# Performance work log

Measured on AMD Instinct MI355X. Metric: run time of the kernel, lower is better.

Reference implementation:

```python
import jax, jax.numpy as jnp
import numpy as np

N_NODES = 50000
N_HYPEREDGES = 10000
N_INC = 800000  # incidences (edges in the bipartite node-hyperedge graph)
D = 128
NEG_SLOPE = 0.2


def segment_softmax(logits, seg, num_segments):
    # numerically stable softmax within segments (grouped by seg)
    m = jax.ops.segment_max(logits, seg, num_segments=num_segments)
    e = jnp.exp(logits - m[seg])
    s = jax.ops.segment_sum(e, seg, num_segments=num_segments)
    return e / s[seg]


def safe_inv(d):
    return jnp.where(d > 0, 1.0 / d, 0.0)


def setup_inputs() -> dict:
    key = jax.random.key(0)
    ks = jax.random.split(key, 8)
    x = jax.random.normal(ks[0], (N_NODES, D), dtype=jnp.float32)
    idx0 = jax.random.randint(ks[1], (N_INC,), 0, N_NODES)          # node ids
    idx1 = jax.random.randint(ks[2], (N_INC,), 0, N_HYPEREDGES)     # hyperedge ids
    hyperedge_index = jnp.stack([idx0, idx1], axis=0).astype(jnp.int64)
    hyperedge_weight = jnp.ones((N_HYPEREDGES,), dtype=jnp.float32)
    sc = 1.0 / np.sqrt(D)
    W_lin = jax.random.normal(ks[3], (D, D), dtype=jnp.float32) * sc
    W_lin2 = jax.random.normal(ks[4], (D, D), dtype=jnp.float32) * sc
    W_lin3 = jax.random.normal(ks[5], (D, D), dtype=jnp.float32) * sc
    att = jax.random.normal(ks[6], (1, 1, 2 * D), dtype=jnp.float32) * sc
    att2 = jax.random.normal(ks[7], (1, 1, 2 * D), dtype=jnp.float32) * sc
    return {"x": x, "hyperedge_index": hyperedge_index,
            "hyperedge_weight": hyperedge_weight,
            "W_lin": W_lin, "W_lin2": W_lin2, "W_lin3": W_lin3,
            "att": att, "att2": att2}


def reference(x, hyperedge_index, hyperedge_weight, W_lin, W_lin2, W_lin3, att, att2):
    N, M = N_NODES, N_HYPEREDGES
    H, F = 1, D
    idx0 = hyperedge_index[0]  # node side  [E]
    idx1 = hyperedge_index[1]  # hyperedge side [E]

    # Hyperedge(): mean-style aggregation of node features into hyperedges
    ones_e = jnp.ones_like(idx1, dtype=x.dtype)
    Binv = safe_inv(jax.ops.segment_sum(ones_e, idx1, num_segments=M))  # [M]
    he0 = jax.ops.segment_sum(x[idx0], idx1, num_segments=M) * Binv[:, None]  # [M,D]

    # linear projections
    xl = (x @ W_lin).reshape(N, H, F)      # [N,H,F]
    hl = (he0 @ W_lin2).reshape(M, H, F)   # [M,H,F]

    # first attention: node-gathered vs hyperedge-gathered, softmax grouped by node
    x_i = xl[idx0]                          # [E,H,F]
    x_j = hl[idx1]                          # [E,H,F]
    alpha = (jnp.concatenate([x_i, x_j], axis=-1) * att).sum(-1)  # [E,H]
    alpha = jax.nn.leaky_relu(alpha, NEG_SLOPE)
    alpha = segment_softmax(alpha, idx0, N)

    # degree normalizations
    Dinv = safe_inv(jax.ops.segment_sum(hyperedge_weight[idx1], idx0, num_segments=N))  # [N]

    # propagate node -> hyperedge: out_e[e] = sum Binv[e]*alpha*x[node]
    msg1 = Binv[idx1][:, None, None] * alpha[:, :, None] * x_i  # [E,H,F]
    out_e = jax.ops.segment_sum(msg1, idx1, num_segments=M)     # [M,H,F]

    # second attention with lin3-transformed hyperedge features
    he2 = (out_e.reshape(M, H * F) @ W_lin3).reshape(M, H, F)
    x_j2 = he2[idx1]
    alpha2 = (jnp.concatenate([x_i, x_j2], axis=-1) * att2).sum(-1)  # [E,H]
    alpha2 = jax.nn.leaky_relu(alpha2, NEG_SLOPE)
    alpha2 = segment_softmax(alpha2, idx0, N)

    # propagate hyperedge -> node: out_n[n] = sum Dinv[n]*alpha2*out_e[hyperedge]
    msg2 = Dinv[idx0][:, None, None] * alpha2[:, :, None] * out_e[idx1]  # [E,H,F]
    out_n = jax.ops.segment_sum(msg2, idx0, num_segments=N)              # [N,H,F]

    return out_n.reshape(N, H * F)
```

## Files before the change

kernel.cpp:

```cpp
#include <hip/hip_runtime.h>
#include <math.h>

#define DF 128
#define TILE 8192
#define CAPA 8192
#define CAPB 10240
typedef unsigned int uint;
typedef __attribute__((ext_vector_type(8))) short bf16x8;
typedef __attribute__((ext_vector_type(4))) float f32x4;

__device__ __forceinline__ float leaky(float s){ return s > 0.f ? s : 0.2f*s; }

__device__ __forceinline__ uint bfr(float f){
    uint u = __float_as_uint(f);
    return (u + 0x7fffu + ((u >> 16) & 1u)) >> 16;
}
__device__ __forceinline__ uint bf2(float a, float b){ return bfr(a) | (bfr(b) << 16); }
__device__ __forceinline__ float blo(uint v){ return __uint_as_float(v << 16); }
__device__ __forceinline__ float bhi(uint v){ return __uint_as_float(v & 0xffff0000u); }

__device__ __forceinline__ uint fenc(float f){
    uint u = __float_as_uint(f);
    return (u & 0x80000000u) ? ~u : (u | 0x80000000u);
}
__device__ __forceinline__ float fdec(uint k){
    return (k & 0x80000000u) ? __uint_as_float(k ^ 0x80000000u) : __uint_as_float(~k);
}

__device__ __forceinline__ void load_edge(const void* raw, int is64, int E, int e,
                                          int& n, int& m){
    if (is64){
        const long long* p = (const long long*)raw;
        n = (int)p[e]; m = (int)p[(long long)E + e];
    } else {
        const int* p = (const int*)raw;
        n = p[e]; m = p[E + e];
    }
}

__global__ __launch_bounds__(256) void prep(
        const uint* __restrict__ raw, int* __restrict__ ctrl,
        int* __restrict__ gcurA, int* __restrict__ gcurB,
        const float* __restrict__ W1, const float* __restrict__ W2,
        const float* __restrict__ W3,
        const float* __restrict__ att, const float* __restrict__ att2,
        float* __restrict__ w2a, float* __restrict__ v1,
        float* __restrict__ v2, float* __restrict__ v3,
        uint* __restrict__ W1t, int E)
{
    int t = threadIdx.x;
    int bid = blockIdx.x;
    if (bid == 0){
        __shared__ int cnt;
        gcurA[t] = t*CAPA;
        gcurB[t] = t*CAPB;
        if (t == 0){ cnt = 0; ctrl[1] = 0; ctrl[2] = 0; }
        __syncthreads();
        int nz = 0;
        for (int i = 0; i < 4; i++){
            int w = 2*(t*4 + i) + 1;
            if (w < 2*E) nz += (raw[w] != 0u);
        }
        atomicAdd(&cnt, nz);
        __syncthreads();
        if (t == 0) ctrl[0] = (cnt == 0) ? 1 : 0;
    } else if (bid == 1){
        int d = t & 127;
        const float* W = (t < 128) ? W2 : W1;
        const float* a = (t < 128) ? (att + 128) : att;
        float s = 0.f;
        for (int f = 0; f < 128; f++) s += W[d*128 + f]*a[f];
        if (t < 128) w2a[d] = s; else v1[d] = s;
    } else if (bid == 2){
        __shared__ float sw3a[128];
        int d = t & 127;
        const float* W = (t < 128) ? W1 : W3;
        const float* a = (t < 128) ? att2 : (att2 + 128);
        float s = 0.f;
        for (int f = 0; f < 128; f++) s += W[d*128 + f]*a[f];
        if (t < 128) v2[d] = s; else sw3a[d] = s;
        __syncthreads();
        if (t < 128){
            float s2 = 0.f;
            for (int f = 0; f < 128; f++) s2 += W1[t*128 + f]*sw3a[f];
            v3[t] = s2;
        }
    } else {
        int base = (bid - 3)*1024;
        for (int p = base + t; p < base + 1024; p += 256){
            int f = p >> 6, dh = p & 63;
            W1t[p] = bf2(W1[(2*dh)*128 + f], W1[(2*dh + 1)*128 + f]);
        }
    }
}

__global__ __launch_bounds__(512) void scatter_gemm(
        const void* __restrict__ raw, const int* __restrict__ ctrl,
        int* __restrict__ gcurA, int* __restrict__ gcurB,
        uint* __restrict__ bktA, uint* __restrict__ bktB,
        const float* __restrict__ X, const uint* __restrict__ W1t,
        const float* __restrict__ w2a, const float* __restrict__ v1,
        const float* __restrict__ v2, const float* __restrict__ v3,
        uint* __restrict__ xlb, float* __restrict__ a1x, float* __restrict__ a2x,
        float* __restrict__ px, float* __restrict__ pxl,
        int E, int N, int SC)
{
    __shared__ char smem[73728];
    int t = threadIdx.x;
    int bid = blockIdx.x;

    if (bid < SC){
        uint* stA = (uint*)smem;
        uint* stB = (uint*)(smem + 32768);
        int*  hA  = (int*)(smem + 65536);
        int*  scA = hA + 256; int* cuA = hA + 512; int* bA = hA + 768;
        int*  hB  = hA + 1024; int* scB = hA + 1280; int* cuB = hA + 1536; int* bB = hA + 1792;
        if (t < 256){ hA[t] = 0; hB[t] = 0; }
        __syncthreads();
        int tb = bid*TILE;
        int cnt = min(TILE, E - tb);
        int is64 = ctrl[0];
        for (int i = t; i < cnt; i += 512){
            int n, m; load_edge(raw, is64, E, tb + i, n, m);
            atomicAdd(&hA[n >> 8], 1);
            atomicAdd(&hB[m >> 6], 1);
        }
        __syncthreads();
        if (t < 256){ scA[t] = hA[t]; scB[t] = hB[t]; }
        __syncthreads();
        for (int off = 1; off < 256; off <<= 1){
            int vA = 0, vB = 0;
            if (t < 256 && t >= off){ vA = scA[t - off]; vB = scB[t - off]; }
            __syncthreads();
            if (t < 256){ scA[t] += vA; scB[t] += vB; }
            __syncthreads();
        }
        if (t < 256){
            scA[t] -= hA[t]; scB[t] -= hB[t];
            cuA[t] = scA[t]; cuB[t] = scB[t];
            bA[t] = atomicAdd(&gcurA[t], hA[t]);
            bB[t] = atomicAdd(&gcurB[t], hB[t]);
        }
        __syncthreads();
        for (int i = t; i < cnt; i += 512){
            int n, m; load_edge(raw, is64, E, tb + i, n, m);
            int pA = atomicAdd(&cuA[n >> 8], 1);
            stA[pA] = ((uint)n << 14) | (uint)m;
            int pB = atomicAdd(&cuB[m >> 6], 1);
            stB[pB] = ((uint)m << 16) | (uint)n;
        }
        __syncthreads();
        for (int p = t; p < cnt; p += 512){
            uint v = stA[p]; int b = (int)(v >> 22);
            bktA[bA[b] + (p - scA[b])] = v;
            uint w = stB[p]; int c = (int)(w >> 22);
            bktB[bB[c] + (p - scB[c])] = w;
        }
    } else {
        char* lds = smem;
        int lane = t & 63, wv = t >> 6;
        int row0 = (bid - SC)*128;
        {
            const uint4* g = (const uint4*)W1t;
            #pragma unroll
            for (int i = 0; i < 4; i++){
                int u = i*512 + t;
                int col = u >> 4;
                uint4 v = g[u];
                *(uint4*)(lds + 32768 + ((u*16) ^ ((col & 7) << 4))) = v;
            }
        }
        {
            int cg = t & 31;
            float4 c_px = ((const float4*)w2a)[cg];
            float4 c_a1 = ((const float4*)v1 )[cg];
            float4 c_a2 = ((const float4*)v2 )[cg];
            float4 c_pl = ((const float4*)v3 )[cg];
            #pragma unroll
            for (int i = 0; i < 8; i++){
                int idx = i*512 + t;
                int rl = idx >> 5;
                int row = row0 + rl;
                float4 xv = make_float4(0.f, 0.f, 0.f, 0.f);
                if (row < N) xv = ((const float4*)X)[(size_t)row*32 + cg];
                uint2 pk; pk.x = bf2(xv.x, xv.y); pk.y = bf2(xv.z, xv.w);
                *(uint2*)(lds + rl*256 + ((cg*8) ^ ((rl & 7) << 4))) = pk;
                float d0 = xv.x*c_px.x + xv.y*c_px.y + xv.z*c_px.z + xv.w*c_px.w;
                float d1 = xv.x*c_a1.x + xv.y*c_a1.y + xv.z*c_a1.z + xv.w*c_a1.w;
                float d2 = xv.x*c_a2.x + xv.y*c_a2.y + xv.z*c_a2.z + xv.w*c_a2.w;
                float d3 = xv.x*c_pl.x + xv.y*c_pl.y + xv.z*c_pl.z + xv.w*c_pl.w;
                #pragma unroll
                for (int off = 16; off > 0; off >>= 1){
                    d0 += __shfl_xor(d0, off); d1 += __shfl_xor(d1, off);
                    d2 += __shfl_xor(d2, off); d3 += __shfl_xor(d3, off);
                }
                if (cg == 0 && row < N){
                    px[row] = d0; a1x[row] = d1; a2x[row] = d2; pxl[row] = d3;
                }
            }
        }
        __syncthreads();
        f32x4 acc[8];
        #pragma unroll
        for (int i = 0; i < 8; i++) acc[i] = (f32x4){0.f, 0.f, 0.f, 0.f};
        int arow = wv*16 + (lane & 15);
        int aswz = (arow & 7) << 4;
        int bswz = (lane & 7) << 4;
        #pragma unroll
        for (int ks = 0; ks < 4; ks++){
            int au16 = ((lane >> 4) + ks*4)*16;
            bf16x8 af = *(const bf16x8*)(lds + arow*256 + (au16 ^ aswz));
            #pragma unroll
            for (int nf = 0; nf < 8; nf++){
                int bcol = nf*16 + (lane & 15);
                bf16x8 bf = *(const bf16x8*)(lds + 32768 + bcol*256 + (au16 ^ bswz));
                acc[nf] = __builtin_amdgcn_mfma_f32_16x16x32_bf16(af, bf, acc[nf], 0, 0, 0);
            }
        }
        __syncthreads();
        #pragma unroll
        for (int nf = 0; nf < 8; nf++){
            #pragma unroll
            for (int reg = 0; reg < 4; reg++){
                int rl = wv*16 + (lane >> 4)*4 + reg;
                int col = nf*16 + (lane & 15);
                *(unsigned short*)(lds + rl*256 + ((col*2) ^ ((rl & 7) << 4))) =
                    (unsigned short)bfr(acc[nf][reg]);
            }
        }
        __syncthreads();
        #pragma unroll
        for (int j = 0; j < 4; j++){
            int unit = j*64 + lane;
            int rl = wv*16 + (unit >> 4);
            int uu = unit & 15;
            uint4 v = *(const uint4*)(lds + rl*256 + ((uu*16) ^ ((rl & 7) << 4)));
            int grow = row0 + rl;
            if (grow < N) ((uint4*)xlb)[(size_t)grow*16 + uu] = v;
        }
    }
}

__global__ __launch_bounds__(256) void csr_edge(
        const uint* __restrict__ bktB, const int* __restrict__ gcurB,
        int* __restrict__ adj1, int2* __restrict__ rg1,
        const float* __restrict__ px, float* __restrict__ a1h,
        uint* __restrict__ g1key, int M)
{
    __shared__ int h[64], sc[64], cu[64];
    __shared__ float fsum[64];
    int t = threadIdx.x;
    int b = blockIdx.x;
    int sb = b*CAPB;
    int total = gcurB[b] - sb;
    int kb = b << 6;
    if (t < 64){ h[t] = 0; fsum[t] = 0.f; }
    __syncthreads();
    const uint* src = bktB + sb;
    for (int i = t; i < total; i += 256)
        atomicAdd(&h[(int)(src[i] >> 16) - kb], 1);
    __syncthreads();
    if (t < 64) sc[t] = h[t];
    __syncthreads();
    for (int off = 1; off < 64; off <<= 1){
        int v = (t < 64 && t >= off) ? sc[t - off] : 0;
        __syncthreads();
        if (t < 64) sc[t] += v;
        __syncthreads();
    }
    if (t < 64){ sc[t] -= h[t]; cu[t] = sc[t]; }
    __syncthreads();
    for (int i = t; i < total; i += 256){
        uint v = src[i];
        int k = (int)(v >> 16) - kb;
        int pos = atomicAdd(&cu[k], 1);
        int n = (int)(v & 0xFFFFu);
        adj1[sb + pos] = n;
        atomicAdd(&fsum[k], px[n]);
    }
    __syncthreads();
    if (t < 64){
        int key = kb + t;
        float av = -3.4e38f;
        if (key < M){
            av = (h[t] > 0) ? fsum[t]/(float)h[t] : 0.f;
            rg1[key] = make_int2(sb + sc[t], sb + sc[t] + h[t]);
            a1h[key] = av;
        }
        #pragma unroll
        for (int off = 32; off > 0; off >>= 1)
            av = fmaxf(av, __shfl_xor(av, off));
        if (t == 0) atomicMax(g1key, fenc(av));
    }
}

__global__ __launch_bounds__(256) void csr_node(
        const uint* __restrict__ bktA, const int* __restrict__ gcurA,
        int* __restrict__ adj0, int2* __restrict__ rg0,
        const float* __restrict__ a1x, const float* __restrict__ a1h,
        const float* __restrict__ hw, const float* __restrict__ pxl,
        const uint* __restrict__ g1key, uint* __restrict__ g2key,
        float4* __restrict__ pk1, float* __restrict__ Dinv, int N)
{
    __shared__ int h[256], sc[256], cu[256];
    __shared__ uint sm[CAPA];
    __shared__ float wmax[4];
    int t = threadIdx.x;
    int b = blockIdx.x;
    int sb = b*CAPA;
    int total = gcurA[b] - sb;
    int kb = b << 8;
    float G1 = fdec(*g1key);
    h[t] = 0;
    __syncthreads();
    const uint* src = bktA + sb;
    for (int i = t; i < total; i += 256)
        atomicAdd(&h[(int)(src[i] >> 14) - kb], 1);
    __syncthreads();
    sc[t] = h[t];
    __syncthreads();
    for (int off = 1; off < 256; off <<= 1){
        int v = (t >= off) ? sc[t - off] : 0;
        __syncthreads();
        sc[t] += v;
        __syncthreads();
    }
    sc[t] -= h[t];
    cu[t] = sc[t];
    __syncthreads();
    for (int i = t; i < total; i += 256){
        uint v = src[i];
        int k = (int)(v >> 14) - kb;
        int pos = atomicAdd(&cu[k], 1);
        sm[pos] = v & 0x3FFFu;
    }
    __syncthreads();
    for (int i = t; i < total; i += 256) adj0[sb + i] = (int)sm[i];
    int key = kb + t;
    float pl = (key < N) ? pxl[key] : 0.f;
    if (key < N){
        int deg = h[t], beg = sc[t];
        rg0[key] = make_int2(sb + beg, sb + beg + deg);
        float ax = a1x[key];
        float mx = leaky(ax + G1);
        float se = 0.f, wsum = 0.f;
        for (int j = 0; j < deg; j++){
            int m = (int)sm[beg + j];
            wsum += hw[m];
            se += expf(leaky(ax + a1h[m]) - mx);
        }
        pk1[key] = make_float4(ax, mx, (deg > 0) ? 1.f/se : 0.f, pl);
        Dinv[key] = (wsum > 0.f) ? 1.f/wsum : 0.f;
    }
    float pv = pl;
    #pragma unroll
    for (int off = 32; off > 0; off >>= 1) pv = fmaxf(pv, __shfl_xor(pv, off));
    if ((t & 63) == 0) wmax[t >> 6] = pv;
    __syncthreads();
    if (t == 0){
        float bm = fmaxf(fmaxf(wmax[0], wmax[1]), fmaxf(wmax[2], wmax[3]));
        atomicMax(g2key, fenc(fmaxf(bm, 0.f)));
    }
}

__global__ __launch_bounds__(256) void agg_oute(
    const int2* __restrict__ rg1, const int* __restrict__ adj1,
    const float4* __restrict__ pk1, const float* __restrict__ a1h,
    const uint* __restrict__ xlb, uint* __restrict__ outeb,
    float* __restrict__ a2h, int M)
{
    __shared__ float part[2][132];
    int t = threadIdx.x;
    int wv = t >> 6, lane = t & 63;
    int slot = wv >> 1, half = wv & 1;
    int m = blockIdx.x*2 + slot;
    int sub = lane >> 4, cg = lane & 15;
    const uint4* x4p = (const uint4*)xlb;
    float acc[8] = {0,0,0,0,0,0,0,0};
    float sca = 0.f;
    float binv = 0.f;
    if (m < M){
        int2 r = rg1[m];
        int b = r.x, e = r.y, deg = e - b;
        binv = deg > 0 ? 1.f/(float)deg : 0.f;
        float ah = a1h[m];
        int hl = (deg + 1) >> 1;
        int hb = b + half*hl;
        int he = min(e, hb + hl);
        for (int base = hb; base < he; base += 64){
            int cnt = min(64, he - base);
            int n = 0; float al = 0.f;
            if (lane < cnt){
                n = adj1[base + lane];
                float4 g = pk1[n];
                al = expf(leaky(g.x + ah) - g.y) * g.z;
                sca += al * g.w;
            }
            int t4 = 0;
            for (; t4 + 8 <= cnt; t4 += 8){
                int   nb0 = __shfl(n,  t4 + sub);
                float ab0 = __shfl(al, t4 + sub);
                int   nb1 = __shfl(n,  t4 + 4 + sub);
                float ab1 = __shfl(al, t4 + 4 + sub);
                uint4 v0 = x4p[(size_t)nb0*16 + cg];
                uint4 v1 = x4p[(size_t)nb1*16 + cg];
                acc[0] += ab0*blo(v0.x); acc[1] += ab0*bhi(v0.x);
                acc[2] += ab0*blo(v0.y); acc[3] += ab0*bhi(v0.y);
                acc[4] += ab0*blo(v0.z); acc[5] += ab0*bhi(v0.z);
                acc[6] += ab0*blo(v0.w); acc[7] += ab0*bhi(v0.w);
                acc[0] += ab1*blo(v1.x); acc[1] += ab1*bhi(v1.x);
                acc[2] += ab1*blo(v1.y); acc[3] += ab1*bhi(v1.y);
                acc[4] += ab1*blo(v1.z); acc[5] += ab1*bhi(v1.z);
                acc[6] += ab1*blo(v1.w); acc[7] += ab1*bhi(v1.w);
            }
            for (; t4 < cnt; t4 += 4){
                int   nb = __shfl(n,  t4 + sub);
                float ab = __shfl(al, t4 + sub);
                uint4 v = x4p[(size_t)nb*16 + cg];
                acc[0] += ab*blo(v.x); acc[1] += ab*bhi(v.x);
                acc[2] += ab*blo(v.y); acc[3] += ab*bhi(v.y);
                acc[4] += ab*blo(v.z); acc[5] += ab*bhi(v.z);
                acc[6] += ab*blo(v.w); acc[7] += ab*bhi(v.w);
            }
        }
        #pragma unroll
        for (int i = 0; i < 8; i++){
            acc[i] += __shfl_xor(acc[i], 32);
            acc[i] += __shfl_xor(acc[i], 16);
        }
        #pragma unroll
        for (int off = 32; off > 0; off >>= 1) sca += __shfl_xor(sca, off);
    }
    if (half == 1 && lane < 16){
        #pragma unroll
        for (int i = 0; i < 8; i++) part[slot][cg*8 + i] = acc[i];
        if (lane == 0) part[slot][128] = sca;
    }
    __syncthreads();
    if (half == 0 && m < M && lane < 16){
        uint4 w;
        w.x = bf2(binv*(acc[0] + part[slot][cg*8+0]), binv*(acc[1] + part[slot][cg*8+1]));
        w.y = bf2(binv*(acc[2] + part[slot][cg*8+2]), binv*(acc[3] + part[slot][cg*8+3]));
        w.z = bf2(binv*(acc[4] + part[slot][cg*8+4]), binv*(acc[5] + part[slot][cg*8+5]));
        w.w = bf2(binv*(acc[6] + part[slot][cg*8+6]), binv*(acc[7] + part[slot][cg*8+7]));
        ((uint4*)outeb)[(size_t)m*16 + cg] = w;
        if (lane == 0) a2h[m] = binv*(sca + part[slot][128]);
    }
}

__global__ __launch_bounds__(256) void agg_outn(
    const int2* __restrict__ rg0, const int* __restrict__ adj0,
    const float* __restrict__ a2x, const float* __restrict__ a2h,
    const float* __restrict__ Dinv, const uint* __restrict__ outeb,
    const uint* __restrict__ g2key, float* __restrict__ out, int N)
{
    int n = blockIdx.x*4 + (threadIdx.x >> 6);
    int lane = threadIdx.x & 63;
    if (n >= N) return;
    int2 r = rg0[n];
    int b = r.x, e = r.y;
    float ax = a2x[n];
    float mx = leaky(ax + fdec(*g2key));
    int sub = lane >> 4, cg = lane & 15;
    const uint4* o4p = (const uint4*)outeb;
    float acc[8] = {0,0,0,0,0,0,0,0};
    float sa = 0.f;
    for (int base = b; base < e; base += 64){
        int cnt = min(64, e - base);
        int m = 0; float al = 0.f;
        if (lane < cnt){
            m = adj0[base + lane];
            al = expf(leaky(ax + a2h[m]) - mx);
            sa += al;
        }
        int t4 = 0;
        for (; t4 + 8 <= cnt; t4 += 8){
            int   mb0 = __shfl(m,  t4 + sub);
            float ab0 = __shfl(al, t4 + sub);
            int   mb1 = __shfl(m,  t4 + 4 + sub);
            float ab1 = __shfl(al, t4 + 4 + sub);
            uint4 v0 = o4p[(size_t)mb0*16 + cg];
            uint4 v1 = o4p[(size_t)mb1*16 + cg];
            acc[0] += ab0*blo(v0.x); acc[1] += ab0*bhi(v0.x);
            acc[2] += ab0*blo(v0.y); acc[3] += ab0*bhi(v0.y);
            acc[4] += ab0*blo(v0.z); acc[5] += ab0*bhi(v0.z);
            acc[6] += ab0*blo(v0.w); acc[7] += ab0*bhi(v0.w);
            acc[0] += ab1*blo(v1.x); acc[1] += ab1*bhi(v1.x);
            acc[2] += ab1*blo(v1.y); acc[3] += ab1*bhi(v1.y);
            acc[4] += ab1*blo(v1.z); acc[5] += ab1*bhi(v1.z);
            acc[6] += ab1*blo(v1.w); acc[7] += ab1*bhi(v1.w);
        }
        for (; t4 < cnt; t4 += 4){
            int   mb = __shfl(m,  t4 + sub);
            float ab = __shfl(al, t4 + sub);
            uint4 v = o4p[(size_t)mb*16 + cg];
            acc[0] += ab*blo(v.x); acc[1] += ab*bhi(v.x);
            acc[2] += ab*blo(v.y); acc[3] += ab*bhi(v.y);
            acc[4] += ab*blo(v.z); acc[5] += ab*bhi(v.z);
            acc[6] += ab*blo(v.w); acc[7] += ab*bhi(v.w);
        }
    }
    #pragma unroll
    for (int off = 32; off > 0; off >>= 1) sa += __shfl_xor(sa, off);
    #pragma unroll
    for (int i = 0; i < 8; i++){
        acc[i] += __shfl_xor(acc[i], 32);
        acc[i] += __shfl_xor(acc[i], 16);
    }
    float scale = (sa > 0.f) ? Dinv[n]/sa : 0.f;
    if (lane < 16){
        float4 o0 = make_float4(scale*acc[0], scale*acc[1], scale*acc[2], scale*acc[3]);
        float4 o1 = make_float4(scale*acc[4], scale*acc[5], scale*acc[6], scale*acc[7]);
        ((float4*)out)[(size_t)n*32 + cg*2]     = o0;
        ((float4*)out)[(size_t)n*32 + cg*2 + 1] = o1;
    }
}

extern "C" void kernel_launch(void* const* d_in, const int* in_sizes, int n_in,
                              void* d_out, int out_size, void* d_ws, size_t ws_size,
                              hipStream_t stream){
    const float* x    = (const float*)d_in[0];
    const void*  hidx = d_in[1];
    const float* hw   = (const float*)d_in[2];
    const float* W1   = (const float*)d_in[3];
    const float* W2   = (const float*)d_in[4];
    const float* W3   = (const float*)d_in[5];
    const float* att  = (const float*)d_in[6];
    const float* att2 = (const float*)d_in[7];
    float* out = (float*)d_out;

    const int N = in_sizes[0] / DF;
    const int E = in_sizes[1] / 2;
    const int M = in_sizes[2];

    char* ws = (char*)d_ws;
    size_t o = 0;
    auto take = [&](size_t bytes) -> char* {
        char* p = ws + o;
        o += (bytes + 255) & ~(size_t)255;
        return p;
    };
    const int nbA = (N + 255) >> 8;
    const int nbB = (M + 63) >> 6;

    uint*   xlb  = (uint*)  take((size_t)N*64*4);
    uint*   outeb= (uint*)  take((size_t)M*64*4);
    float*  a1x  = (float*) take((size_t)N*4);
    float*  a2x  = (float*) take((size_t)N*4);
    float*  px   = (float*) take((size_t)N*4);
    float*  pxl  = (float*) take((size_t)N*4);
    float*  Dinv = (float*) take((size_t)N*4);
    float*  a1h  = (float*) take((size_t)M*4);
    float*  a2h  = (float*) take((size_t)M*4);
    float4* pk1  = (float4*)take((size_t)N*16);
    float*  w2a  = (float*) take(DF*4);
    float*  v1   = (float*) take(DF*4);
    float*  v2   = (float*) take(DF*4);
    float*  v3   = (float*) take(DF*4);
    uint*   W1t  = (uint*)  take(128*64*4);
    int2*   rg0  = (int2*)  take((size_t)N*8);
    int2*   rg1  = (int2*)  take((size_t)M*8);
    int*    gcurA= (int*)   take(256*4);
    int*    gcurB= (int*)   take(256*4);
    uint*   bktA = (uint*)  take((size_t)nbA*CAPA*4 + TILE*4);
    uint*   bktB = (uint*)  take((size_t)nbB*CAPB*4 + TILE*4);
    int*    adj0 = (int*)   take((size_t)nbA*CAPA*4);
    int*    adj1 = (int*)   take((size_t)nbB*CAPB*4);
    int*    ctrl = (int*)   take(256);

    const int SC = (E + TILE - 1)/TILE;
    const int GB = (N + 127)/128;

    prep<<<11, 256, 0, stream>>>((const uint*)hidx, ctrl, gcurA, gcurB,
                                 W1, W2, W3, att, att2, w2a, v1, v2, v3, W1t, E);
    scatter_gemm<<<SC + GB, 512, 0, stream>>>(hidx, ctrl, gcurA, gcurB,
                                 bktA, bktB, x, W1t, w2a, v1, v2, v3,
                                 xlb, a1x, a2x, px, pxl, E, N, SC);
    csr_edge<<<nbB, 256, 0, stream>>>(bktB, gcurB, adj1, rg1, px, a1h,
                                      (uint*)&ctrl[1], M);
    csr_node<<<nbA, 256, 0, stream>>>(bktA, gcurA, adj0, rg0,
                                      a1x, a1h, hw, pxl, (uint*)&ctrl[1],
                                      (uint*)&ctrl[2], pk1, Dinv, N);
    agg_oute<<<(M + 1)/2, 256, 0, stream>>>(rg1, adj1, pk1, a1h, xlb, outeb,
                                            a2h, M);
    agg_outn<<<(N + 3)/4, 256, 0, stream>>>(rg0, adj0, a2x, a2h, Dinv, outeb,
                                            (uint*)&ctrl[2], out, N);
}
```

Before: 123.4 us.

## Fuse hyperedge and node CSR build kernels with a ticket-based grid spin wait

Merges the two CSR construction kernels into one launch. The first nbB blocks build the hyperedge CSR and bump a global ticket counter, while the remaining blocks build the node CSR in parallel and spin-wait on the ticket only before the softmax pass that needs a1h and the global max. This removes one kernel launch boundary and lets the node-side bucketing overlap with the edge-side work. Control words are moved to separate cache lines. It relies on all edge blocks being scheduled before or alongside waiting blocks, which is only safe if the grid fits co-resident or the blocks are dispatched in order.

```diff
diff --git a/kernel.cpp b/kernel.cpp
--- a/kernel.cpp
+++ b/kernel.cpp
@@ -54,7 +54,7 @@
         __shared__ int cnt;
         gcurA[t] = t*CAPA;
         gcurB[t] = t*CAPB;
-        if (t == 0){ cnt = 0; ctrl[1] = 0; ctrl[2] = 0; }
+        if (t == 0){ cnt = 0; ctrl[16] = 0; ctrl[32] = 0; ctrl[48] = 0; }
         __syncthreads();
         int nz = 0;
         for (int i = 0; i < 4; i++){
@@ -241,125 +241,134 @@
     }
 }
 
-__global__ __launch_bounds__(256) void csr_edge(
+__global__ __launch_bounds__(256) void csr_fused(
         const uint* __restrict__ bktB, const int* __restrict__ gcurB,
         int* __restrict__ adj1, int2* __restrict__ rg1,
         const float* __restrict__ px, float* __restrict__ a1h,
-        uint* __restrict__ g1key, int M)
-{
-    __shared__ int h[64], sc[64], cu[64];
-    __shared__ float fsum[64];
-    int t = threadIdx.x;
-    int b = blockIdx.x;
-    int sb = b*CAPB;
-    int total = gcurB[b] - sb;
-    int kb = b << 6;
-    if (t < 64){ h[t] = 0; fsum[t] = 0.f; }
-    __syncthreads();
-    const uint* src = bktB + sb;
-    for (int i = t; i < total; i += 256)
-        atomicAdd(&h[(int)(src[i] >> 16) - kb], 1);
-    __syncthreads();
-    if (t < 64) sc[t] = h[t];
-    __syncthreads();
-    for (int off = 1; off < 64; off <<= 1){
-        int v = (t < 64 && t >= off) ? sc[t - off] : 0;
-        __syncthreads();
-        if (t < 64) sc[t] += v;
-        __syncthreads();
-    }
-    if (t < 64){ sc[t] -= h[t]; cu[t] = sc[t]; }
-    __syncthreads();
-    for (int i = t; i < total; i += 256){
-        uint v = src[i];
-        int k = (int)(v >> 16) - kb;
-        int pos = atomicAdd(&cu[k], 1);
-        int n = (int)(v & 0xFFFFu);
-        adj1[sb + pos] = n;
-        atomicAdd(&fsum[k], px[n]);
-    }
-    __syncthreads();
-    if (t < 64){
-        int key = kb + t;
-        float av = -3.4e38f;
-        if (key < M){
-            av = (h[t] > 0) ? fsum[t]/(float)h[t] : 0.f;
-            rg1[key] = make_int2(sb + sc[t], sb + sc[t] + h[t]);
-            a1h[key] = av;
-        }
-        #pragma unroll
-        for (int off = 32; off > 0; off >>= 1)
-            av = fmaxf(av, __shfl_xor(av, off));
-        if (t == 0) atomicMax(g1key, fenc(av));
-    }
-}
-
-__global__ __launch_bounds__(256) void csr_node(
+        uint* __restrict__ g1key,
         const uint* __restrict__ bktA, const int* __restrict__ gcurA,
         int* __restrict__ adj0, int2* __restrict__ rg0,
-        const float* __restrict__ a1x, const float* __restrict__ a1h,
-        const float* __restrict__ hw, const float* __restrict__ pxl,
-        const uint* __restrict__ g1key, uint* __restrict__ g2key,
-        float4* __restrict__ pk1, float* __restrict__ Dinv, int N)
+        const float* __restrict__ a1x, const float* __restrict__ hw,
+        const float* __restrict__ pxl, uint* __restrict__ g2key,
+        float4* __restrict__ pk1, float* __restrict__ Dinv,
+        int* __restrict__ ticket, int N, int M, int nbB)
 {
     __shared__ int h[256], sc[256], cu[256];
     __shared__ uint sm[CAPA];
+    __shared__ float fsum[64];
     __shared__ float wmax[4];
+    __shared__ float sG1;
     int t = threadIdx.x;
-    int b = blockIdx.x;
-    int sb = b*CAPA;
-    int total = gcurA[b] - sb;
-    int kb = b << 8;
-    float G1 = fdec(*g1key);
-    h[t] = 0;
-    __syncthreads();
-    const uint* src = bktA + sb;
-    for (int i = t; i < total; i += 256)
-        atomicAdd(&h[(int)(src[i] >> 14) - kb], 1);
-    __syncthreads();
-    sc[t] = h[t];
-    __syncthreads();
-    for (int off = 1; off < 256; off <<= 1){
-        int v = (t >= off) ? sc[t - off] : 0;
-        __syncthreads();
-        sc[t] += v;
-        __syncthreads();
-    }
-    sc[t] -= h[t];
-    cu[t] = sc[t];
-    __syncthreads();
-    for (int i = t; i < total; i += 256){
-        uint v = src[i];
-        int k = (int)(v >> 14) - kb;
-        int pos = atomicAdd(&cu[k], 1);
-        sm[pos] = v & 0x3FFFu;
-    }
-    __syncthreads();
-    for (int i = t; i < total; i += 256) adj0[sb + i] = (int)sm[i];
-    int key = kb + t;
-    float pl = (key < N) ? pxl[key] : 0.f;
-    if (key < N){
+
+    if (blockIdx.x < nbB){
+        int b = blockIdx.x;
+        int sb = b*CAPB;
+        int total = gcurB[b] - sb;
+        int kb = b << 6;
+        if (t < 64){ h[t] = 0; fsum[t] = 0.f; }
+        __syncthreads();
+        const uint* src = bktB + sb;
+        for (int i = t; i < total; i += 256)
+            atomicAdd(&h[(int)(src[i] >> 16) - kb], 1);
+        __syncthreads();
+        if (t < 64) sc[t] = h[t];
+        __syncthreads();
+        for (int off = 1; off < 64; off <<= 1){
+            int v = (t < 64 && t >= off) ? sc[t - off] : 0;
+            __syncthreads();
+            if (t < 64) sc[t] += v;
+            __syncthreads();
+        }
+        if (t < 64){ sc[t] -= h[t]; cu[t] = sc[t]; }
+        __syncthreads();
+        for (int i = t; i < total; i += 256){
+            uint v = src[i];
+            int k = (int)(v >> 16) - kb;
+            int pos = atomicAdd(&cu[k], 1);
+            int n = (int)(v & 0xFFFFu);
+            adj1[sb + pos] = n;
+            atomicAdd(&fsum[k], px[n]);
+        }
+        __syncthreads();
+        if (t < 64){
+            int key = kb + t;
+            float av = -3.4e38f;
+            if (key < M){
+                av = (h[t] > 0) ? fsum[t]/(float)h[t] : 0.f;
+                rg1[key] = make_int2(sb + sc[t], sb + sc[t] + h[t]);
+                a1h[key] = av;
+            }
+            #pragma unroll
+            for (int off = 32; off > 0; off >>= 1)
+                av = fmaxf(av, __shfl_xor(av, off));
+            if (t == 0) atomicMax(g1key, fenc(av));
+        }
+        __threadfence();
+        __syncthreads();
+        if (t == 0) atomicAdd(ticket, 1);
+    } else {
+        int b = blockIdx.x - nbB;
+        int sb = b*CAPA;
+        int total = gcurA[b] - sb;
+        int kb = b << 8;
+        h[t] = 0;
+        __syncthreads();
+        const uint* src = bktA + sb;
+        for (int i = t; i < total; i += 256)
+            atomicAdd(&h[(int)(src[i] >> 14) - kb], 1);
+        __syncthreads();
+        sc[t] = h[t];
+        __syncthreads();
+        for (int off = 1; off < 256; off <<= 1){
+            int v = (t >= off) ? sc[t - off] : 0;
+            __syncthreads();
+            sc[t] += v;
+            __syncthreads();
+        }
+        sc[t] -= h[t];
+        cu[t] = sc[t];
+        __syncthreads();
+        for (int i = t; i < total; i += 256){
+            uint v = src[i];
+            int k = (int)(v >> 14) - kb;
+            int pos = atomicAdd(&cu[k], 1);
+            sm[pos] = v & 0x3FFFu;
+        }
+        __syncthreads();
+        for (int i = t; i < total; i += 256) adj0[sb + i] = (int)sm[i];
+        int key = kb + t;
         int deg = h[t], beg = sc[t];
-        rg0[key] = make_int2(sb + beg, sb + beg + deg);
-        float ax = a1x[key];
-        float mx = leaky(ax + G1);
-        float se = 0.f, wsum = 0.f;
-        for (int j = 0; j < deg; j++){
-            int m = (int)sm[beg + j];
-            wsum += hw[m];
-            se += expf(leaky(ax + a1h[m]) - mx);
-        }
-        pk1[key] = make_float4(ax, mx, (deg > 0) ? 1.f/se : 0.f, pl);
-        Dinv[key] = (wsum > 0.f) ? 1.f/wsum : 0.f;
-    }
-    float pv = pl;
-    #pragma unroll
-    for (int off = 32; off > 0; off >>= 1) pv = fmaxf(pv, __shfl_xor(pv, off));
-    if ((t & 63) == 0) wmax[t >> 6] = pv;
-    __syncthreads();
-    if (t == 0){
-        float bm = fmaxf(fmaxf(wmax[0], wmax[1]), fmaxf(wmax[2], wmax[3]));
-        atomicMax(g2key, fenc(fmaxf(bm, 0.f)));
+        if (key < N) rg0[key] = make_int2(sb + beg, sb + beg + deg);
+        float pl = (key < N) ? pxl[key] : 0.f;
+        float pv = pl;
+        #pragma unroll
+        for (int off = 32; off > 0; off >>= 1) pv = fmaxf(pv, __shfl_xor(pv, off));
+        if ((t & 63) == 0) wmax[t >> 6] = pv;
+        __syncthreads();
+        if (t == 0){
+            float bm = fmaxf(fmaxf(wmax[0], wmax[1]), fmaxf(wmax[2], wmax[3]));
+            atomicMax(g2key, fenc(fmaxf(bm, 0.f)));
+        }
+        if (t == 0){
+            while (__atomic_load_n((volatile int*)ticket, __ATOMIC_RELAXED) < nbB)
+                __builtin_amdgcn_s_sleep(16);
+            __threadfence();
+            sG1 = fdec(__atomic_load_n((volatile uint*)g1key, __ATOMIC_RELAXED));
+        }
+        __syncthreads();
+        float G1 = sG1;
+        if (key < N){
+            float ax = a1x[key];
+            float mx = leaky(ax + G1);
+            float se = 0.f, wsum = 0.f;
+            for (int j = 0; j < deg; j++){
+                int m = (int)sm[beg + j];
+                wsum += hw[m];
+                se += expf(leaky(ax + a1h[m]) - mx);
+            }
+            pk1[key] = make_float4(ax, mx, (deg > 0) ? 1.f/se : 0.f, pl);
+            Dinv[key] = (wsum > 0.f) ? 1.f/wsum : 0.f;
+        }
     }
 }
 
@@ -576,13 +585,13 @@
     scatter_gemm<<<SC + GB, 512, 0, stream>>>(hidx, ctrl, gcurA, gcurB,
                                  bktA, bktB, x, W1t, w2a, v1, v2, v3,
                                  xlb, a1x, a2x, px, pxl, E, N, SC);
-    csr_edge<<<nbB, 256, 0, stream>>>(bktB, gcurB, adj1, rg1, px, a1h,
-                                      (uint*)&ctrl[1], M);
-    csr_node<<<nbA, 256, 0, stream>>>(bktA, gcurA, adj0, rg0,
-                                      a1x, a1h, hw, pxl, (uint*)&ctrl[1],
-                                      (uint*)&ctrl[2], pk1, Dinv, N);
+    csr_fused<<<nbB + nbA, 256, 0, stream>>>(bktB, gcurB, adj1, rg1, px, a1h,
+                                 (uint*)&ctrl[16],
+                                 bktA, gcurA, adj0, rg0, a1x, hw, pxl,
+                                 (uint*)&ctrl[48], pk1, Dinv, &ctrl[32],
+                                 N, M, nbB);
     agg_oute<<<(M + 1)/2, 256, 0, stream>>>(rg1, adj1, pk1, a1h, xlb, outeb,
                                             a2h, M);
     agg_outn<<<(N + 3)/4, 256, 0, stream>>>(rg0, adj0, a2x, a2h, Dinv, outeb,
-                                            (uint*)&ctrl[2], out, N);
-}
+                                            (uint*)&ctrl[48], out, N);
+}
```

New measurement: 151.2 us. +22.5%, slower.
